# Optimization experiments

Hardware: AMD Instinct MI355X
Metric: run time of the kernel (lower is better)

The kernel has to match this reference:

```python
import jax, jax.numpy as jnp
import numpy as np

B, S, H, D = 4, 4096, 1024, 64

def setup_inputs() -> dict:
    key = jax.random.key(0)
    ks = jax.random.split(key, 10)
    return {
        "query": jax.random.normal(ks[0], (B, S, H), jnp.float32),
        "key": jax.random.normal(ks[1], (B, S, H), jnp.float32),
        "value": jax.random.normal(ks[2], (B, S, H), jnp.float32),
        "mask": jax.random.randint(ks[3], (B, S), 0, 2, jnp.int32),
        "Wq": jax.random.normal(ks[4], (H, D), jnp.float32) * 0.02,
        "bq": jax.random.normal(ks[5], (D,), jnp.float32) * 0.02,
        "Wk": jax.random.normal(ks[6], (H, D), jnp.float32) * 0.02,
        "bk": jax.random.normal(ks[7], (D,), jnp.float32) * 0.02,
        "Wv": jax.random.normal(ks[8], (H, D), jnp.float32) * 0.02,
        "bv": jax.random.normal(ks[9], (D,), jnp.float32) * 0.02,
    }

def reference(query, key, value, mask, Wq, bq, Wk, bk, Wv, bv):
    # single-head projections: [B,S,H] @ [H,D] -> [B,S,D]
    q = query @ Wq + bq
    k = key @ Wk + bk
    v = value @ Wv + bv
    scale = 1.0 / np.sqrt(D).astype(np.float32)
    # [B,Sq,Sk] score matrix (faithful to the unfused original)
    scores = jnp.einsum('bqd,bkd->bqk', q, k) * scale
    # mask [B,Sk] broadcast over query dim; masked positions -> -1e9
    scores = jnp.where(mask[:, None, :] == 0, jnp.float32(-1e9), scores)
    att = jax.nn.softmax(scores, axis=-1)
    # dropout prob = 0.0 -> identity
    return jnp.einsum('bqk,bkd->bqd', att, v)
```

## Files before the change

### kernel.cpp

```cpp
#include <hip/hip_runtime.h>
#include <hip/hip_bf16.h>
#include <stdint.h>


typedef __bf16 bf16;
typedef __bf16 bf16x8 __attribute__((ext_vector_type(8)));
typedef float f32x16 __attribute__((ext_vector_type(16)));

union B8 { uint4 u; bf16x8 v; uint32_t w[4]; };

#define AS1 __attribute__((address_space(1)))
#define AS3 __attribute__((address_space(3)))

__device__ __forceinline__ void async16(const void* g, void* l) {
  __builtin_amdgcn_global_load_lds((AS1 void*)(g), (AS3 void*)(l), 16, 0, 0);
}

#define KSC 0.18033688011112042f

__global__ void setup_kernel(const float* __restrict__ Wq, const float* __restrict__ Wk,
                             const float* __restrict__ Wv, const int* __restrict__ mask,
                             bf16* __restrict__ wT, float* __restrict__ biasArr)
{
  int item = blockIdx.x * 256 + threadIdx.x;
  if (item < 24576) {
    int mat = item >> 13;
    int rem = item & 8191;
    int n   = rem >> 7;
    int c   = rem & 127;
    int kt  = c >> 3;
    int cl  = c & 7;
    const float* W = (mat == 0) ? Wq : (mat == 1) ? Wk : Wv;
    int kbase = kt * 64 + cl * 8;
    union { bf16 b[8]; uint4 u; } pk;
    #pragma unroll
    for (int j = 0; j < 8; ++j)
      pk.b[j] = (bf16)W[(kbase + j) * 64 + n];
    bf16* o = wT + mat * 65536;
    *(uint4*)(o + n * 1024 + kt * 64 + ((cl ^ (n & 7)) << 3)) = pk.u;
  } else {
    int i = (item - 24576) << 2;
    const int4 m = *(const int4*)(mask + i);
    float4 b;
    b.x = m.x ? 0.0f : -1e30f;
    b.y = m.y ? 0.0f : -1e30f;
    b.z = m.z ? 0.0f : -1e30f;
    b.w = m.w ? 0.0f : -1e30f;
    *(float4*)(biasArr + i) = b;
  }
}

__global__ __launch_bounds__(256, 4) void proj_kernel(
    const float* __restrict__ Xq, const float* __restrict__ Xk, const float* __restrict__ Xv,
    const bf16* __restrict__ wT,
    const float* __restrict__ bq, const float* __restrict__ bk, const float* __restrict__ bv,
    bf16* __restrict__ qo, bf16* __restrict__ ko, bf16* __restrict__ vTo)
{
  const int bx = blockIdx.x;
  const int mat = bx >> 7;
  const int m0 = (bx & 127) << 7;
  const float* X    = (mat == 0) ? Xq : (mat == 1) ? Xk : Xv;
  const float* bias = (mat == 0) ? bq : (mat == 1) ? bk : bv;
  const bf16* w = wT + mat * 65536;

  __shared__ __align__(16) bf16 xs[128 * 64];
  __shared__ __align__(16) bf16 ws[64 * 64];

  const int tid = threadIdx.x;
  const int lane = tid & 63;
  const int wv = tid >> 6;
  const int half = lane >> 5;
  const int ln = lane & 31;

  f32x16 acc0 = {};
  f32x16 acc1 = {};

  for (int kc = 0; kc < 1024; kc += 64) {
    __syncthreads();
    #pragma unroll
    for (int p = 0; p < 8; ++p) {
      int id = p * 256 + tid;
      int r = id >> 4;
      int c4 = (id & 15) << 2;
      float4 f = *(const float4*)(X + (size_t)(m0 + r) * 1024 + kc + c4);
      int phys = (c4 >> 3) ^ (r & 7);
      union { bf16 b[4]; uint2 u; } pk;
      pk.b[0] = (bf16)f.x; pk.b[1] = (bf16)f.y; pk.b[2] = (bf16)f.z; pk.b[3] = (bf16)f.w;
      *(uint2*)(xs + r * 64 + phys * 8 + (c4 & 7)) = pk.u;
    }
    #pragma unroll
    for (int p = 0; p < 2; ++p) {
      int id = p * 256 + tid;
      int n = id >> 3;
      int c = id & 7;
      *(uint4*)(ws + n * 64 + c * 8) = *(const uint4*)(w + n * 1024 + kc + c * 8);
    }
    __syncthreads();
    #pragma unroll
    for (int s = 0; s < 4; ++s) {
      int am = (wv << 5) + ln;
      B8 a;  a.u  = *(const uint4*)(xs + am * 64 + (((2 * s + half) ^ (am & 7)) << 3));
      B8 b0; b0.u = *(const uint4*)(ws + ln * 64 + (((2 * s + half) ^ (ln & 7)) << 3));
      int n1 = ln + 32;
      B8 b1; b1.u = *(const uint4*)(ws + n1 * 64 + (((2 * s + half) ^ (n1 & 7)) << 3));
      acc0 = __builtin_amdgcn_mfma_f32_32x32x16_bf16(a.v, b0.v, acc0, 0, 0, 0);
      acc1 = __builtin_amdgcn_mfma_f32_32x32x16_bf16(a.v, b1.v, acc1, 0, 0, 0);
    }
  }
  __syncthreads();
  {
    float bias0 = bias[ln];
    float bias1 = bias[ln + 32];
    #pragma unroll
    for (int r = 0; r < 16; ++r) {
      int mrow = (wv << 5) + (r & 3) + ((r >> 2) << 3) + (half << 2);
      xs[mrow * 64 + ln]      = (bf16)(acc0[r] + bias0);
      xs[mrow * 64 + ln + 32] = (bf16)(acc1[r] + bias1);
    }
  }
  __syncthreads();
  if (mat < 2) {
    bf16* gout = (mat == 0) ? qo : ko;
    #pragma unroll
    for (int p = 0; p < 4; ++p) {
      int id = p * 256 + tid;
      int r = id >> 3;
      int c = id & 7;
      int phys = c ^ (r & 7);
      *(uint4*)(gout + (size_t)(m0 + r) * 64 + phys * 8) = *(const uint4*)(xs + r * 64 + c * 8);
    }
  } else {
    int batch = m0 >> 12;
    int s0 = m0 & 4095;
    #pragma unroll
    for (int p = 0; p < 4; ++p) {
      int id = p * 256 + tid;
      int d  = id >> 4;
      int ck = id & 15;
      int tk = ck >> 3;
      int cl = ck & 7;
      union { bf16 b[8]; uint4 u; } pk;
      #pragma unroll
      for (int j = 0; j < 8; ++j) pk.b[j] = xs[(tk * 64 + cl * 8 + j) * 64 + d];
      int phys = cl ^ (d & 7);
      *(uint4*)(vTo + ((size_t)batch * 64 + d) * 4096 + s0 + tk * 64 + phys * 8) = pk.u;
    }
  }
}

__global__ __launch_bounds__(256, 2) void flash_kernel(
    const bf16* __restrict__ qb, const bf16* __restrict__ kb, const bf16* __restrict__ vT,
    const float* __restrict__ biasArr, float* __restrict__ out)
{
  __shared__ __align__(16) char smem[65536];
  bf16* ksb = (bf16*)smem;
  bf16* vsb = (bf16*)(smem + 32768);

  const int tid = threadIdx.x;
  const int lane = tid & 63;
  const int wv = tid >> 6;
  const int half = lane >> 5;
  const int ln = lane & 31;

  const int batch = blockIdx.x >> 6;
  const int q0 = (blockIdx.x & 63) << 6;

  bf16x8 qf[2][4];
  const bf16* qbase = qb + ((size_t)batch * 4096 + q0) * 64;
  #pragma unroll
  for (int qk = 0; qk < 2; ++qk)
  #pragma unroll
  for (int s = 0; s < 4; ++s) {
    int qq = (qk << 5) + ln;
    int phys = (2 * s + half) ^ (qq & 7);
    B8 t; t.u = *(const uint4*)(qbase + qq * 64 + phys * 8);
    qf[qk][s] = t.v;
  }

  f32x16 acc[2][2] = {{{}, {}}, {{}, {}}};
  float den0 = 0.f, den1 = 0.f;

  bf16* kds = ksb + wv * 4096;
  bf16* vds = vsb + wv * 4096;
  const bf16* kgb = kb + (size_t)batch * 4096 * 64;
  const bf16* vgb = vT + (size_t)batch * 64 * 4096;
  const float* barr = biasArr + batch * 4096;

  for (int it = 0; it < 16; ++it) {
    const int key0 = wv * 1024 + it * 64;
    __syncthreads();
    const bf16* ksrc = kgb + (size_t)key0 * 64;
    #pragma unroll
    for (int i = 0; i < 8; ++i)
      async16((const char*)ksrc + i * 1024 + lane * 16, (char*)kds + i * 1024);
    const bf16* vsrc = vgb + key0;
    #pragma unroll
    for (int i = 0; i < 8; ++i)
      async16((const char*)vsrc + ((size_t)(i * 8 + (lane >> 3)) * 4096 + (lane & 7) * 8) * 2,
              (char*)vds + i * 1024);
    __syncthreads();

    #pragma unroll
    for (int st = 0; st < 2; ++st) {
      f32x16 s0 = {};
      f32x16 s1 = {};
      #pragma unroll
      for (int s = 0; s < 4; ++s) {
        int key = (st << 5) + ln;
        B8 af; af.u = *(const uint4*)(kds + key * 64 + (((2 * s + half) ^ (key & 7)) << 3));
        s0 = __builtin_amdgcn_mfma_f32_32x32x16_bf16(af.v, qf[0][s], s0, 0, 0, 0);
        s1 = __builtin_amdgcn_mfma_f32_32x32x16_bf16(af.v, qf[1][s], s1, 0, 0, 0);
      }
      float bb[16];
      #pragma unroll
      for (int g = 0; g < 4; ++g)
        *(float4*)&bb[4 * g] = *(const float4*)(barr + key0 + (st << 5) + 8 * g + (half << 2));
      uint32_t pk0[8], pk1[8];
      #pragma unroll
      for (int i = 0; i < 8; ++i) {
        float a0 = __builtin_amdgcn_exp2f(fmaf(s0[2 * i],     KSC, bb[2 * i]));
        float a1 = __builtin_amdgcn_exp2f(fmaf(s0[2 * i + 1], KSC, bb[2 * i + 1]));
        float c0 = __builtin_amdgcn_exp2f(fmaf(s1[2 * i],     KSC, bb[2 * i]));
        float c1 = __builtin_amdgcn_exp2f(fmaf(s1[2 * i + 1], KSC, bb[2 * i + 1]));
        den0 += a0 + a1;
        den1 += c0 + c1;
        union { bf16 b[2]; uint32_t u; } u0, u1;
        u0.b[0] = (bf16)a0; u0.b[1] = (bf16)a1;
        u1.b[0] = (bf16)c0; u1.b[1] = (bf16)c1;
        pk0[i] = u0.u; pk1[i] = u1.u;
      }
      uint32_t xp0[8], xp1[8];
      #pragma unroll
      for (int i = 0; i < 8; ++i) {
        xp0[i] = (uint32_t)__shfl_xor((int)pk0[i], 32);
        xp1[i] = (uint32_t)__shfl_xor((int)pk1[i], 32);
      }
      #pragma unroll
      for (int t = 0; t < 2; ++t) {
        B8 p0f, p1f;
        p0f.w[0] = half ? xp0[4 * t + 2] : pk0[4 * t];
        p0f.w[1] = half ? xp0[4 * t + 3] : pk0[4 * t + 1];
        p0f.w[2] = half ? pk0[4 * t + 2] : xp0[4 * t];
        p0f.w[3] = half ? pk0[4 * t + 3] : xp0[4 * t + 1];
        p1f.w[0] = half ? xp1[4 * t + 2] : pk1[4 * t];
        p1f.w[1] = half ? xp1[4 * t + 3] : pk1[4 * t + 1];
        p1f.w[2] = half ? pk1[4 * t + 2] : xp1[4 * t];
        p1f.w[3] = half ? pk1[4 * t + 3] : xp1[4 * t + 1];
        #pragma unroll
        for (int dh = 0; dh < 2; ++dh) {
          int d = (dh << 5) + ln;
          B8 vf; vf.u = *(const uint4*)(vds + d * 64 +
                          ((((st << 2) + (t << 1) + half) ^ (d & 7)) << 3));
          acc[0][dh] = __builtin_amdgcn_mfma_f32_32x32x16_bf16(vf.v, p0f.v, acc[0][dh], 0, 0, 0);
          acc[1][dh] = __builtin_amdgcn_mfma_f32_32x32x16_bf16(vf.v, p1f.v, acc[1][dh], 0, 0, 0);
        }
      }
    }
  }

  den0 += __shfl_xor(den0, 32);
  den1 += __shfl_xor(den1, 32);

  float* nb = (float*)smem;
  float* dn = (float*)(smem + 34816);

  __syncthreads();
  if (wv >= 2) {
    float* mynb = nb + (wv - 2) * 4352;
    #pragma unroll
    for (int qk = 0; qk < 2; ++qk)
    #pragma unroll
    for (int dh = 0; dh < 2; ++dh)
    #pragma unroll
    for (int g = 0; g < 4; ++g) {
      int q = (qk << 5) + ln;
      int d = 8 * g + (half << 2) + (dh << 5);
      f32x16 a = acc[qk][dh];
      *(float4*)(mynb + q * 68 + d) = make_float4(a[4*g], a[4*g+1], a[4*g+2], a[4*g+3]);
    }
    if (half == 0) {
      dn[(wv - 2) * 64 + ln]      = den0;
      dn[(wv - 2) * 64 + 32 + ln] = den1;
    }
  }
  __syncthreads();
  if (wv < 2) {
    float* pb = nb + wv * 4352;
    #pragma unroll
    for (int qk = 0; qk < 2; ++qk)
    #pragma unroll
    for (int dh = 0; dh < 2; ++dh)
    #pragma unroll
    for (int g = 0; g < 4; ++g) {
      int q = (qk << 5) + ln;
      int d = 8 * g + (half << 2) + (dh << 5);
      float4 t = *(const float4*)(pb + q * 68 + d);
      acc[qk][dh][4*g+0] += t.x; acc[qk][dh][4*g+1] += t.y;
      acc[qk][dh][4*g+2] += t.z; acc[qk][dh][4*g+3] += t.w;
    }
    den0 += dn[wv * 64 + ln];
    den1 += dn[wv * 64 + 32 + ln];
  }
  __syncthreads();
  if (wv < 2) {
    float* mynb = nb + wv * 4352;
    #pragma unroll
    for (int qk = 0; qk < 2; ++qk)
    #pragma unroll
    for (int dh = 0; dh < 2; ++dh)
    #pragma unroll
    for (int g = 0; g < 4; ++g) {
      int q = (qk << 5) + ln;
      int d = 8 * g + (half << 2) + (dh << 5);
      f32x16 a = acc[qk][dh];
      *(float4*)(mynb + q * 68 + d) = make_float4(a[4*g], a[4*g+1], a[4*g+2], a[4*g+3]);
    }
    if (half == 0) {
      dn[wv * 64 + ln]      = den0;
      dn[wv * 64 + 32 + ln] = den1;
    }
  }
  __syncthreads();
  #pragma unroll
  for (int p = 0; p < 4; ++p) {
    int i = p * 256 + tid;
    int qq = i >> 4;
    int d4 = (i & 15) << 2;
    float4 A = *(const float4*)(nb + qq * 68 + d4);
    float4 Bv = *(const float4*)(nb + 4352 + qq * 68 + d4);
    float dd = dn[qq] + dn[64 + qq];
    float inv = 1.0f / dd;
    float4 o = make_float4((A.x + Bv.x) * inv, (A.y + Bv.y) * inv,
                           (A.z + Bv.z) * inv, (A.w + Bv.w) * inv);
    *(float4*)(out + ((size_t)batch * 4096 + q0 + qq) * 64 + d4) = o;
  }
}

extern "C" void kernel_launch(void* const* d_in, const int* in_sizes, int n_in,
                              void* d_out, int out_size, void* d_ws, size_t ws_size,
                              hipStream_t stream)
{
  const float* query = (const float*)d_in[0];
  const float* key   = (const float*)d_in[1];
  const float* value = (const float*)d_in[2];
  const int*   mask  = (const int*)d_in[3];
  const float* Wq    = (const float*)d_in[4];
  const float* bq    = (const float*)d_in[5];
  const float* Wk    = (const float*)d_in[6];
  const float* bk    = (const float*)d_in[7];
  const float* Wv    = (const float*)d_in[8];
  const float* bv    = (const float*)d_in[9];
  float* out = (float*)d_out;

  bf16* qb = (bf16*)d_ws;
  bf16* kb = qb + 1048576;
  bf16* vT = kb + 1048576;
  bf16* wT = vT + 1048576;
  float* biasArr = (float*)((char*)d_ws + 3 * 2097152 + 393216);

  setup_kernel<<<112, 256, 0, stream>>>(Wq, Wk, Wv, mask, wT, biasArr);
  proj_kernel<<<384, 256, 0, stream>>>(query, key, value, wT, bq, bk, bv, qb, kb, vT);
  flash_kernel<<<256, 256, 0, stream>>>(qb, kb, vT, biasArr, out);
}
```

Measured before the change: 265.9 us.

## Load projection operands directly into registers with double-buffered prefetch, drop LDS staging

The projection kernel now uses single-wave blocks of 32 rows. Each lane loads its X row segment and weight columns straight from global memory into registers, with a two-chunk software prefetch. The LDS tiling and per-chunk barriers are removed, and the weight layout drops its swizzle so it matches the direct loads. The cost is redundant weight reads across many blocks, uncoalesced strided global loads, and a much larger launch of small blocks.

```diff
diff --git a/kernel.cpp b/kernel.cpp
--- a/kernel.cpp
+++ b/kernel.cpp
@@ -28,16 +28,13 @@
     int rem = item & 8191;
     int n   = rem >> 7;
     int c   = rem & 127;
-    int kt  = c >> 3;
-    int cl  = c & 7;
     const float* W = (mat == 0) ? Wq : (mat == 1) ? Wk : Wv;
-    int kbase = kt * 64 + cl * 8;
     union { bf16 b[8]; uint4 u; } pk;
     #pragma unroll
     for (int j = 0; j < 8; ++j)
-      pk.b[j] = (bf16)W[(kbase + j) * 64 + n];
+      pk.b[j] = (bf16)W[(c * 8 + j) * 64 + n];
     bf16* o = wT + mat * 65536;
-    *(uint4*)(o + n * 1024 + kt * 64 + ((cl ^ (n & 7)) << 3)) = pk.u;
+    *(uint4*)(o + n * 1024 + c * 8) = pk.u;
   } else {
     int i = (item - 24576) << 2;
     const int4 m = *(const int4*)(mask + i);
@@ -50,100 +47,113 @@
   }
 }
 
-__global__ __launch_bounds__(256, 4) void proj_kernel(
+struct PF {
+  float4 xa[4], xb[4];
+  uint4  wa[4], wb[4];
+};
+
+__device__ __forceinline__ void load_chunk(const float* __restrict__ xr,
+                                           const bf16* __restrict__ w0,
+                                           const bf16* __restrict__ w1,
+                                           int kc, PF& p) {
+  #pragma unroll
+  for (int s = 0; s < 4; ++s) {
+    int k = kc + s * 16;
+    p.xa[s] = *(const float4*)(xr + k);
+    p.xb[s] = *(const float4*)(xr + k + 4);
+    p.wa[s] = *(const uint4*)(w0 + k);
+    p.wb[s] = *(const uint4*)(w1 + k);
+  }
+}
+
+__device__ __forceinline__ void comp_chunk(const PF& p, f32x16& a0, f32x16& a1) {
+  #pragma unroll
+  for (int s = 0; s < 4; ++s) {
+    union { bf16 b[8]; bf16x8 v; } af;
+    af.b[0] = (bf16)p.xa[s].x; af.b[1] = (bf16)p.xa[s].y;
+    af.b[2] = (bf16)p.xa[s].z; af.b[3] = (bf16)p.xa[s].w;
+    af.b[4] = (bf16)p.xb[s].x; af.b[5] = (bf16)p.xb[s].y;
+    af.b[6] = (bf16)p.xb[s].z; af.b[7] = (bf16)p.xb[s].w;
+    B8 wa; wa.u = p.wa[s];
+    B8 wb; wb.u = p.wb[s];
+    a0 = __builtin_amdgcn_mfma_f32_32x32x16_bf16(af.v, wa.v, a0, 0, 0, 0);
+    a1 = __builtin_amdgcn_mfma_f32_32x32x16_bf16(af.v, wb.v, a1, 0, 0, 0);
+  }
+}
+
+__global__ __launch_bounds__(64, 2) void proj_kernel(
     const float* __restrict__ Xq, const float* __restrict__ Xk, const float* __restrict__ Xv,
     const bf16* __restrict__ wT,
     const float* __restrict__ bq, const float* __restrict__ bk, const float* __restrict__ bv,
     bf16* __restrict__ qo, bf16* __restrict__ ko, bf16* __restrict__ vTo)
 {
   const int bx = blockIdx.x;
-  const int mat = bx >> 7;
-  const int m0 = (bx & 127) << 7;
+  const int mat = bx >> 9;
+  const int m0 = (bx & 511) << 5;
   const float* X    = (mat == 0) ? Xq : (mat == 1) ? Xk : Xv;
   const float* bias = (mat == 0) ? bq : (mat == 1) ? bk : bv;
   const bf16* w = wT + mat * 65536;
 
-  __shared__ __align__(16) bf16 xs[128 * 64];
-  __shared__ __align__(16) bf16 ws[64 * 64];
-
-  const int tid = threadIdx.x;
-  const int lane = tid & 63;
-  const int wv = tid >> 6;
+  __shared__ __align__(16) bf16 cs[32 * 64];
+
+  const int lane = threadIdx.x;
   const int half = lane >> 5;
   const int ln = lane & 31;
 
+  const float* xr = X + (size_t)(m0 + ln) * 1024 + half * 8;
+  const bf16*  w0 = w + ln * 1024 + half * 8;
+  const bf16*  w1 = w + (ln + 32) * 1024 + half * 8;
+
   f32x16 acc0 = {};
   f32x16 acc1 = {};
 
-  for (int kc = 0; kc < 1024; kc += 64) {
-    __syncthreads();
-    #pragma unroll
-    for (int p = 0; p < 8; ++p) {
-      int id = p * 256 + tid;
-      int r = id >> 4;
-      int c4 = (id & 15) << 2;
-      float4 f = *(const float4*)(X + (size_t)(m0 + r) * 1024 + kc + c4);
-      int phys = (c4 >> 3) ^ (r & 7);
-      union { bf16 b[4]; uint2 u; } pk;
-      pk.b[0] = (bf16)f.x; pk.b[1] = (bf16)f.y; pk.b[2] = (bf16)f.z; pk.b[3] = (bf16)f.w;
-      *(uint2*)(xs + r * 64 + phys * 8 + (c4 & 7)) = pk.u;
-    }
-    #pragma unroll
-    for (int p = 0; p < 2; ++p) {
-      int id = p * 256 + tid;
-      int n = id >> 3;
-      int c = id & 7;
-      *(uint4*)(ws + n * 64 + c * 8) = *(const uint4*)(w + n * 1024 + kc + c * 8);
-    }
-    __syncthreads();
-    #pragma unroll
-    for (int s = 0; s < 4; ++s) {
-      int am = (wv << 5) + ln;
-      B8 a;  a.u  = *(const uint4*)(xs + am * 64 + (((2 * s + half) ^ (am & 7)) << 3));
-      B8 b0; b0.u = *(const uint4*)(ws + ln * 64 + (((2 * s + half) ^ (ln & 7)) << 3));
-      int n1 = ln + 32;
-      B8 b1; b1.u = *(const uint4*)(ws + n1 * 64 + (((2 * s + half) ^ (n1 & 7)) << 3));
-      acc0 = __builtin_amdgcn_mfma_f32_32x32x16_bf16(a.v, b0.v, acc0, 0, 0, 0);
-      acc1 = __builtin_amdgcn_mfma_f32_32x32x16_bf16(a.v, b1.v, acc1, 0, 0, 0);
-    }
-  }
-  __syncthreads();
+  PF A, Bp;
+  load_chunk(xr, w0, w1, 0, A);
+  for (int c = 0; c < 16; c += 2) {
+    load_chunk(xr, w0, w1, (c + 1) * 64, Bp);
+    comp_chunk(A, acc0, acc1);
+    if (c + 2 < 16) load_chunk(xr, w0, w1, (c + 2) * 64, A);
+    comp_chunk(Bp, acc0, acc1);
+  }
+
   {
-    float bias0 = bias[ln];
-    float bias1 = bias[ln + 32];
+    float b0v = bias[ln];
+    float b1v = bias[ln + 32];
     #pragma unroll
     for (int r = 0; r < 16; ++r) {
-      int mrow = (wv << 5) + (r & 3) + ((r >> 2) << 3) + (half << 2);
-      xs[mrow * 64 + ln]      = (bf16)(acc0[r] + bias0);
-      xs[mrow * 64 + ln + 32] = (bf16)(acc1[r] + bias1);
-    }
-  }
-  __syncthreads();
+      int mrow = (r & 3) + 8 * (r >> 2) + 4 * half;
+      cs[mrow * 64 + ln]      = (bf16)(acc0[r] + b0v);
+      cs[mrow * 64 + ln + 32] = (bf16)(acc1[r] + b1v);
+    }
+  }
+  __syncthreads();
+
   if (mat < 2) {
     bf16* gout = (mat == 0) ? qo : ko;
     #pragma unroll
     for (int p = 0; p < 4; ++p) {
-      int id = p * 256 + tid;
+      int id = p * 64 + lane;
       int r = id >> 3;
       int c = id & 7;
       int phys = c ^ (r & 7);
-      *(uint4*)(gout + (size_t)(m0 + r) * 64 + phys * 8) = *(const uint4*)(xs + r * 64 + c * 8);
+      *(uint4*)(gout + (size_t)(m0 + r) * 64 + phys * 8) = *(const uint4*)(cs + r * 64 + c * 8);
     }
   } else {
     int batch = m0 >> 12;
-    int s0 = m0 & 4095;
+    int sk = m0 & 4095;
+    int tb = sk & ~63;
+    int halfTile = (sk >> 5) & 1;
     #pragma unroll
     for (int p = 0; p < 4; ++p) {
-      int id = p * 256 + tid;
-      int d  = id >> 4;
-      int ck = id & 15;
-      int tk = ck >> 3;
-      int cl = ck & 7;
+      int id = p * 64 + lane;
+      int d = id >> 2;
+      int j = id & 3;
       union { bf16 b[8]; uint4 u; } pk;
       #pragma unroll
-      for (int j = 0; j < 8; ++j) pk.b[j] = xs[(tk * 64 + cl * 8 + j) * 64 + d];
+      for (int t = 0; t < 8; ++t) pk.b[t] = cs[(j * 8 + t) * 64 + d];
+      int cl = halfTile * 4 + j;
       int phys = cl ^ (d & 7);
-      *(uint4*)(vTo + ((size_t)batch * 64 + d) * 4096 + s0 + tk * 64 + phys * 8) = pk.u;
+      *(uint4*)(vTo + ((size_t)batch * 64 + d) * 4096 + tb + phys * 8) = pk.u;
     }
   }
 }
@@ -359,6 +369,6 @@
   float* biasArr = (float*)((char*)d_ws + 3 * 2097152 + 393216);
 
   setup_kernel<<<112, 256, 0, stream>>>(Wq, Wk, Wv, mask, wT, biasArr);
-  proj_kernel<<<384, 256, 0, stream>>>(query, key, value, wT, bq, bk, bv, qb, kb, vT);
+  proj_kernel<<<1536, 64, 0, stream>>>(query, key, value, wT, bq, bk, bv, qb, kb, vT);
   flash_kernel<<<256, 256, 0, stream>>>(qb, kb, vT, biasArr, out);
 }
```

After: 283.8 us. 6.7% more time.
